# Performance work log

Measured on AMD Instinct MI355X. Metric: run time of the kernel, lower is better.

Reference implementation:

```python
import jax, jax.numpy as jnp
import numpy as np

# static config (mirrors init_kwargs)
F_T, S = 8, 24            # video_shape = (F_T, S, S)
K, DIL = 3, 1             # kernel_size, dilation (same for all 3 axes)
HEADS, DHEAD, DIM = 8, 64, 512
INNER = HEADS * DHEAD
PAD = DIL * (K - 1)       # causal: pad 2 at the FRONT of each spatial axis
KJ = K ** 3               # 27 neighbors per query
N_VID = F_T * S * S       # 4608 video tokens


def causal_pad(t):
    # t: [B, D, F, S, S] -> pad front of f/h/w axes (torch F.pad (PAD*?,0) causal layout)
    return jnp.pad(t, ((0, 0), (0, 0), (PAD, 0), (PAD, 0), (PAD, 0)))


def unfold3d(t):
    # torch unfoldNd equivalent. t: [B, D, F+PAD, S+PAD, S+PAD]
    # returns [B, N_VID, KJ, D]; kernel offsets ordered (kf, kh, kw) w fastest,
    # matching torch unfold's channel-major / kernel-minor layout after the
    # rearrange 'b (d j) i -> b i j d'.
    sl = []
    for i in range(K):
        for j in range(K):
            for kk in range(K):
                sl.append(t[:, :, i * DIL:i * DIL + F_T,
                                  j * DIL:j * DIL + S,
                                  kk * DIL:kk * DIL + S])
    u = jnp.stack(sl, axis=2)                      # [B, D, KJ, F, S, S]
    B, D = t.shape[0], t.shape[1]
    u = u.reshape(B, D, KJ, N_VID)
    return jnp.transpose(u, (0, 3, 2, 1))          # [B, N_VID, KJ, D]


def make_mask():
    # True where the neighbor falls into zero padding (out-of-range / future under causal pad)
    ones = jnp.ones((1, 1, F_T, S, S), jnp.float32)
    u = unfold3d(causal_pad(ones))[0, :, :, 0]     # [N_VID, KJ]
    m = u == 0.0
    return jnp.pad(m, ((0, 0), (1, 0)), constant_values=False)  # bos col never masked


def stable_softmax(t, alpha=32.0 ** 2):
    t = t / alpha
    t = t - jax.lax.stop_gradient(jnp.max(t, axis=-1, keepdims=True))
    return jax.nn.softmax(t * alpha, axis=-1)


def setup_inputs() -> dict:
    key = jax.random.key(0)
    ks = jax.random.split(key, 9)
    return {
        "x": jax.random.normal(ks[0], (1, N_VID + 1, DIM), jnp.float32),
        "Wq": jax.random.normal(ks[1], (DIM, INNER), jnp.float32) * 0.02,
        "Wkv": jax.random.normal(ks[2], (DIM, 2 * INNER), jnp.float32) * 0.02,
        "W_th": jax.random.normal(ks[3], (HEADS, HEADS), jnp.float32) * 0.2,
        "Wout": jax.random.normal(ks[4], (INNER, DIM), jnp.float32) * 0.02,
        "bout": jax.random.normal(ks[5], (DIM,), jnp.float32) * 0.02,
        "ax1": jax.random.normal(ks[6], (K, HEADS), jnp.float32),
        "ax2": jax.random.normal(ks[7], (K, HEADS), jnp.float32),
        "ax3": jax.random.normal(ks[8], (K, HEADS), jnp.float32),
    }


def reference(x, Wq, Wkv, W_th, Wout, bout, ax1, ax2, ax3):
    b, n, _ = x.shape                       # b=1, n = 1 + N_VID (no extra padding)
    h, d = HEADS, DHEAD
    scale = d ** -0.5

    q = x @ Wq
    k, v = jnp.split(x @ Wkv, 2, axis=-1)

    def to_heads(t):  # 'b n (h d) -> (b h) n d'
        return t.reshape(b, n, h, d).transpose(0, 2, 1, 3).reshape(b * h, n, d)

    q, k, v = map(to_heads, (q, k, v))
    q = q[:, 1:] * scale                    # drop bos query
    k_bos, v_bos = k[:, :1], v[:, :1]       # [bh, 1, d]
    k, v = k[:, 1:], v[:, 1:]

    def to_vid(t):  # 'b (f h w) d -> b d f h w'
        return t.reshape(b * h, F_T, S, S, d).transpose(0, 4, 1, 2, 3)

    ku = unfold3d(causal_pad(to_vid(k)))    # [bh, N, KJ, d]
    vu = unfold3d(causal_pad(to_vid(v)))
    N = ku.shape[1]

    kb = jnp.broadcast_to(k_bos[:, :, None, :], (b * h, N, 1, d))
    vb = jnp.broadcast_to(v_bos[:, :, None, :], (b * h, N, 1, d))
    ku = jnp.concatenate([kb, ku], axis=2)  # [bh, N, KJ+1, d]
    vu = jnp.concatenate([vb, vu], axis=2)

    sim = jnp.einsum('bid,bijd->bij', q, ku)                 # [bh, N, KJ+1]

    # axial relative position bias over the 3x3x3 kernel, pad 0 for bos column
    rel = (ax1[:, None, None, :] + ax2[None, :, None, :] + ax3[None, None, :, :])
    rel = rel.reshape(KJ, h)                                 # [27, h]
    bias = jnp.pad(rel.T[:, None, :], ((0, 0), (0, 0), (1, 0)))  # [h, 1, KJ+1]

    sim = sim.reshape(b, h, N, KJ + 1) + bias[None]
    mask = make_mask()                                       # [N, KJ+1]
    sim = jnp.where(mask[None, None], -jnp.finfo(sim.dtype).max, sim)

    attn = stable_softmax(sim)                               # [b, h, N, KJ+1]
    attn = jnp.einsum('hg,bgij->bhij', W_th, attn)           # talking heads 1x1 conv

    out = jnp.einsum('bhij,bhijd->bhid', attn, vu.reshape(b, h, N, KJ + 1, d))
    out = jnp.concatenate([v_bos.reshape(b, h, 1, d), out], axis=2)  # re-attach bos value
    out = out.transpose(0, 2, 1, 3).reshape(b, n, h * d)     # '(b h) n d -> b n (h d)'
    return out @ Wout + bout
```

## Files before the change

kernel.cpp:

```cpp
#include <hip/hip_runtime.h>
#include <hip/hip_bf16.h>


constexpr int TFR   = 8;
constexpr int SDIM  = 24;
constexpr int NVID  = TFR * SDIM * SDIM;
constexpr int NTOK  = NVID + 1;
constexpr int NH    = 8;
constexpr int DM    = 512;
constexpr int NJ    = 28;

typedef __attribute__((ext_vector_type(8))) short bf16x8;
typedef __attribute__((ext_vector_type(8))) unsigned short ushort8;
typedef __attribute__((ext_vector_type(4))) float f32x4;

typedef const __attribute__((address_space(1))) unsigned int* gas_ptr;
typedef __attribute__((address_space(3))) unsigned int* las_ptr;

__device__ __forceinline__ float bf2f(unsigned short u) {
    return __uint_as_float((unsigned)u << 16);
}
__device__ __forceinline__ unsigned short f2bf(float f) {
    __hip_bfloat16 h = __float2bfloat16(f);
    return reinterpret_cast<unsigned short&>(h);
}

__global__ __launch_bounds__(256)
void prep_w(const float* __restrict__ Wq, const float* __restrict__ Wkv,
            const float* __restrict__ Wout, const float* __restrict__ x,
            __hip_bfloat16* __restrict__ Wqkvt, __hip_bfloat16* __restrict__ Woutt,
            __hip_bfloat16* __restrict__ xb)
{
    const int tid = threadIdx.x;
    int tb = blockIdx.x;

    if (tb >= 1024) {
        const size_t base = (size_t)(tb - 1024) * 2048 + (size_t)tid * 8;
        if (base < (size_t)NTOK * DM) {
            const float4 f0 = *(const float4*)(x + base);
            const float4 f1 = *(const float4*)(x + base + 4);
            unsigned short v[8] = { f2bf(f0.x), f2bf(f0.y), f2bf(f0.z), f2bf(f0.w),
                                    f2bf(f1.x), f2bf(f1.y), f2bf(f1.z), f2bf(f1.w) };
            *(ushort8*)(xb + base) = *(const ushort8*)v;
        }
        return;
    }

    __shared__ float t[32][33];
    const float* W; __hip_bfloat16* Wt; int Nd, tX, rowOff;
    if (tb < 256)      { W = Wq;   Wt = Wqkvt; Nd = 512;  tX = 16; rowOff = 0;   }
    else if (tb < 768) { tb -= 256; W = Wkv;  Wt = Wqkvt; Nd = 1024; tX = 32; rowOff = 512; }
    else               { tb -= 768; W = Wout; Wt = Woutt; Nd = 512;  tX = 16; rowOff = 0;   }
    const int n0 = (tb % tX) * 32, k0 = (tb / tX) * 32;
    const int r  = tid >> 3;
    const int c4 = (tid & 7) * 4;
    const float4 v = *(const float4*)(W + (size_t)(k0 + r) * Nd + n0 + c4);
    t[r][c4 + 0] = v.x; t[r][c4 + 1] = v.y; t[r][c4 + 2] = v.z; t[r][c4 + 3] = v.w;
    __syncthreads();
    #pragma unroll
    for (int j = 0; j < 4; ++j)
        Wt[(size_t)(rowOff + n0 + r) * 512 + k0 + c4 + j] = __float2bfloat16(t[c4 + j][r]);
}

__global__ __launch_bounds__(256)
void gemm_qkv(const __hip_bfloat16* __restrict__ Ab, const __hip_bfloat16* __restrict__ Bt,
              float* __restrict__ Cq, __hip_bfloat16* __restrict__ Ckv, int M)
{
    constexpr int BM = 128, BN = 128, BK = 64, K = 512;
    __shared__ __align__(16) short As[2][BM * BK];
    __shared__ __align__(16) short Bs[2][BN * BK];

    const int tid  = threadIdx.x;
    const int bid  = blockIdx.x;
    const int xcd  = bid & 7, pos = bid >> 3;
    const int L    = (xcd < 4) ? xcd * 56 + pos : 224 + (xcd - 4) * 55 + pos;
    const int m0   = (L / 12) * BM;
    const int n0   = (L % 12) * BN;

    const int lane = tid & 63;
    const int wave = tid >> 6;
    const int wm   = (wave >> 1) * 64;
    const int wn   = (wave & 1) * 64;
    const int col  = lane & 15;
    const int quad = lane >> 4;

    f32x4 acc[4][4] = {};

    auto stage = [&](int buf, int k0) {
        #pragma unroll
        for (int it = 0; it < 4; ++it) {
            const int idx = it * 256 + tid;
            const int r   = idx >> 3;
            const int u   = (idx & 7) ^ (r & 7);
            const int gm  = (m0 + r < M) ? (m0 + r) : (M - 1);
            const __hip_bfloat16* gp = Ab + (size_t)gm * K + k0 + u * 8;
            __builtin_amdgcn_global_load_lds(
                (gas_ptr)gp, (las_ptr)&As[buf][(it * 256 + wave * 64) * 8], 16, 0, 0);
        }
        #pragma unroll
        for (int it = 0; it < 4; ++it) {
            const int idx = it * 256 + tid;
            const int r   = idx >> 3;
            const int u   = (idx & 7) ^ (r & 7);
            const __hip_bfloat16* gp = Bt + (size_t)(n0 + r) * K + k0 + u * 8;
            __builtin_amdgcn_global_load_lds(
                (gas_ptr)gp, (las_ptr)&Bs[buf][(it * 256 + wave * 64) * 8], 16, 0, 0);
        }
    };

    stage(0, 0);
    __syncthreads();

    #pragma unroll 2
    for (int t = 0; t < K / BK; ++t) {
        const int cur = t & 1;
        if (t + 1 < K / BK) stage(cur ^ 1, (t + 1) * BK);

        #pragma unroll
        for (int ks = 0; ks < 2; ++ks) {
            bf16x8 af[4], bfr[4];
            #pragma unroll
            for (int mt = 0; mt < 4; ++mt) {
                const int r = wm + mt * 16 + col;
                const int u = (ks * 4 + quad) ^ (r & 7);
                af[mt] = *(const bf16x8*)(&As[cur][r * BK + u * 8]);
            }
            #pragma unroll
            for (int nt = 0; nt < 4; ++nt) {
                const int r = wn + nt * 16 + col;
                const int u = (ks * 4 + quad) ^ (r & 7);
                bfr[nt] = *(const bf16x8*)(&Bs[cur][r * BK + u * 8]);
            }
            #pragma unroll
            for (int mt = 0; mt < 4; ++mt)
                #pragma unroll
                for (int nt = 0; nt < 4; ++nt)
                    acc[mt][nt] = __builtin_amdgcn_mfma_f32_16x16x32_bf16(
                        af[mt], bfr[nt], acc[mt][nt], 0, 0, 0);
        }
        __syncthreads();
    }

    const bool isQ = (n0 < 512);
    #pragma unroll
    for (int mt = 0; mt < 4; ++mt) {
        #pragma unroll
        for (int r = 0; r < 4; ++r) {
            const int row = m0 + wm + mt * 16 + quad * 4 + r;
            if (row >= M) continue;
            #pragma unroll
            for (int nt = 0; nt < 4; ++nt) {
                const int cg = n0 + wn + nt * 16 + col;
                const float v = acc[mt][nt][r];
                if (isQ) Cq[(size_t)row * 512 + cg] = v * 0.125f;
                else     Ckv[(size_t)row * 1024 + (cg - 512)] = __float2bfloat16(v);
            }
        }
    }
}

__global__ __launch_bounds__(256)
void gemm_out(const __hip_bfloat16* __restrict__ A, const __hip_bfloat16* __restrict__ Bt,
              float* __restrict__ C, int M, const float* __restrict__ bias)
{
    constexpr int BM = 64, BN = 64, BK = 64, K = 512;
    __shared__ __align__(16) short As[2][BM * BK];
    __shared__ __align__(16) short Bs[2][BN * BK];

    const int tid  = threadIdx.x;
    const int bid  = blockIdx.x;
    const int L    = (bid & 7) * 73 + (bid >> 3);
    const int m0   = (L >> 3) * BM;
    const int n0   = (L & 7) * BN;
    const int lane = tid & 63;
    const int wave = tid >> 6;
    const int wm   = (wave >> 1) * 32;
    const int wn   = (wave & 1) * 32;
    const int col  = lane & 15;
    const int quad = lane >> 4;

    f32x4 acc[2][2] = {};

    auto stage = [&](int buf, int k0) {
        #pragma unroll
        for (int it = 0; it < 2; ++it) {
            const int idx = it * 256 + tid;
            const int r   = idx >> 3;
            const int u   = (idx & 7) ^ (r & 7);
            const int gm  = (m0 + r < M) ? (m0 + r) : (M - 1);
            const __hip_bfloat16* gp = A + (size_t)gm * K + k0 + u * 8;
            __builtin_amdgcn_global_load_lds(
                (gas_ptr)gp, (las_ptr)&As[buf][(it * 256 + wave * 64) * 8], 16, 0, 0);
        }
        #pragma unroll
        for (int it = 0; it < 2; ++it) {
            const int idx = it * 256 + tid;
            const int r   = idx >> 3;
            const int u   = (idx & 7) ^ (r & 7);
            const __hip_bfloat16* gp = Bt + (size_t)(n0 + r) * K + k0 + u * 8;
            __builtin_amdgcn_global_load_lds(
                (gas_ptr)gp, (las_ptr)&Bs[buf][(it * 256 + wave * 64) * 8], 16, 0, 0);
        }
    };

    stage(0, 0);
    __syncthreads();

    #pragma unroll 2
    for (int t = 0; t < K / BK; ++t) {
        const int cur = t & 1;
        if (t + 1 < K / BK) stage(cur ^ 1, (t + 1) * BK);

        #pragma unroll
        for (int ks = 0; ks < 2; ++ks) {
            bf16x8 af[2], bfr[2];
            #pragma unroll
            for (int mt = 0; mt < 2; ++mt) {
                const int r = wm + mt * 16 + col;
                const int u = (ks * 4 + quad) ^ (r & 7);
                af[mt] = *(const bf16x8*)(&As[cur][r * BK + u * 8]);
            }
            #pragma unroll
            for (int nt = 0; nt < 2; ++nt) {
                const int r = wn + nt * 16 + col;
                const int u = (ks * 4 + quad) ^ (r & 7);
                bfr[nt] = *(const bf16x8*)(&Bs[cur][r * BK + u * 8]);
            }
            #pragma unroll
            for (int mt = 0; mt < 2; ++mt)
                #pragma unroll
                for (int nt = 0; nt < 2; ++nt)
                    acc[mt][nt] = __builtin_amdgcn_mfma_f32_16x16x32_bf16(
                        af[mt], bfr[nt], acc[mt][nt], 0, 0, 0);
        }
        __syncthreads();
    }

    #pragma unroll
    for (int mt = 0; mt < 2; ++mt) {
        #pragma unroll
        for (int r = 0; r < 4; ++r) {
            const int row = m0 + wm + mt * 16 + quad * 4 + r;
            if (row >= M) continue;
            #pragma unroll
            for (int nt = 0; nt < 2; ++nt) {
                const int cg = n0 + wn + nt * 16 + col;
                C[(size_t)row * 512 + cg] = acc[mt][nt][r] + bias[cg];
            }
        }
    }
}

__global__ __launch_bounds__(256)
void attn_v2(const float* __restrict__ Q, const __hip_bfloat16* __restrict__ KVb,
             __hip_bfloat16* __restrict__ O,
             const float* __restrict__ W_th,
             const float* __restrict__ ax1, const float* __restrict__ ax2,
             const float* __restrict__ ax3)
{
    __shared__ float attn_s[4][NH * NJ];
    __shared__ float mixed_s[4][NH * NJ];

    const int tid  = threadIdx.x;
    const int wave = tid >> 6;
    const int lane = tid & 63;
    const int g    = lane >> 3;
    const int s    = lane & 7;
    const int bsw  = (blockIdx.x & 7) * (NVID / 4 / 8) + (blockIdx.x >> 3);
    const int i    = __builtin_amdgcn_readfirstlane(bsw * 4 + (tid >> 6));
    const int qrow = i + 1;

    const int t  = i / (SDIM * SDIM);
    const int rm = i % (SDIM * SDIM);
    const int y  = rm / SDIM;
    const int x  = rm % SDIM;

    float qf[8];
    {
        const float4 q0 = *(const float4*)(Q + (size_t)qrow * DM + lane * 8);
        const float4 q1 = *(const float4*)(Q + (size_t)qrow * DM + lane * 8 + 4);
        qf[0] = q0.x; qf[1] = q0.y; qf[2] = q0.z; qf[3] = q0.w;
        qf[4] = q1.x; qf[5] = q1.y; qf[6] = q1.z; qf[7] = q1.w;
    }
    float a1[3], a2[3], a3[3];
    #pragma unroll
    for (int d = 0; d < 3; ++d) {
        a1[d] = ax1[d * NH + g];
        a2[d] = ax2[d * NH + g];
        a3[d] = ax3[d * NH + g];
    }

    float sim[NJ];
    #pragma unroll
    for (int j = 0; j < NJ; ++j) {
        int row; bool valid; float bias;
        if (j == 0) { row = 0; valid = true; bias = 0.f; }
        else {
            const int jp = j - 1;
            const int di = jp / 9, dj = (jp / 3) % 3, dk = jp % 3;
            const int tt = t + di - 2, yy = y + dj - 2, xx = x + dk - 2;
            valid = (tt >= 0) && (yy >= 0) && (xx >= 0);
            row = 1 + tt * SDIM * SDIM + yy * SDIM + xx;
            bias = a1[di] + a2[dj] + a3[dk];
        }
        if (valid) {
            const ushort8 kv = *(const ushort8*)(KVb + (size_t)row * 1024 + lane * 8);
            float p = 0.f;
            #pragma unroll
            for (int e = 0; e < 8; ++e) p += bf2f(kv[e]) * qf[e];
            p += __shfl_xor(p, 1);
            p += __shfl_xor(p, 2);
            p += __shfl_xor(p, 4);
            sim[j] = p + bias;
        } else {
            sim[j] = -1e30f;
        }
    }

    float m = -1e30f;
    #pragma unroll
    for (int j = 0; j < NJ; ++j) m = fmaxf(m, sim[j]);
    float ssum = 0.f;
    #pragma unroll
    for (int j = 0; j < NJ; ++j) { sim[j] = __expf(sim[j] - m); ssum += sim[j]; }
    const float inv = 1.f / ssum;
    #pragma unroll
    for (int j = 0; j < NJ; ++j) sim[j] *= inv;

    if (s == 0) {
        #pragma unroll
        for (int u = 0; u < 7; ++u) {
            f32x4 v4 = { sim[4*u], sim[4*u+1], sim[4*u+2], sim[4*u+3] };
            *(f32x4*)(&attn_s[wave][g * NJ + 4 * u]) = v4;
        }
    }
    __syncthreads();

    if (tid < NH * NJ) {
        const int h = tid / NJ, j = tid % NJ;
        #pragma unroll
        for (int q = 0; q < 4; ++q) {
            float acc = 0.f;
            #pragma unroll
            for (int gg = 0; gg < NH; ++gg)
                acc += W_th[h * NH + gg] * attn_s[q][gg * NJ + j];
            mixed_s[q][h * NJ + j] = acc;
        }
    }
    __syncthreads();

    float acc8[8] = {};
    #pragma unroll
    for (int j = 0; j < NJ; ++j) {
        int row; bool valid;
        if (j == 0) { row = 0; valid = true; }
        else {
            const int jp = j - 1;
            const int di = jp / 9, dj = (jp / 3) % 3, dk = jp % 3;
            const int tt = t + di - 2, yy = y + dj - 2, xx = x + dk - 2;
            valid = (tt >= 0) && (yy >= 0) && (xx >= 0);
            row = 1 + tt * SDIM * SDIM + yy * SDIM + xx;
        }
        if (valid) {
            const ushort8 vv = *(const ushort8*)(KVb + (size_t)row * 1024 + 512 + lane * 8);
            const float w = mixed_s[wave][g * NJ + j];
            #pragma unroll
            for (int e = 0; e < 8; ++e) acc8[e] += w * bf2f(vv[e]);
        }
    }

    unsigned short o[8];
    #pragma unroll
    for (int e = 0; e < 8; ++e) o[e] = f2bf(acc8[e]);
    *(ushort8*)(O + (size_t)qrow * DM + lane * 8) = *(const ushort8*)o;

    if (i == 0) {
        const ushort8 vb = *(const ushort8*)(KVb + 512 + lane * 8);
        *(ushort8*)(O + lane * 8) = vb;
    }
}

extern "C" void kernel_launch(void* const* d_in, const int* in_sizes, int n_in,
                              void* d_out, int out_size, void* d_ws, size_t ws_size,
                              hipStream_t stream)
{
    const float* x    = (const float*)d_in[0];
    const float* Wq   = (const float*)d_in[1];
    const float* Wkv  = (const float*)d_in[2];
    const float* W_th = (const float*)d_in[3];
    const float* Wout = (const float*)d_in[4];
    const float* bout = (const float*)d_in[5];
    const float* ax1  = (const float*)d_in[6];
    const float* ax2  = (const float*)d_in[7];
    const float* ax3  = (const float*)d_in[8];
    float* out = (float*)d_out;

    char* p = (char*)d_ws;
    float* Qf = (float*)p;                       p += (size_t)NTOK * DM * 4;
    __hip_bfloat16* KVb   = (__hip_bfloat16*)p;  p += (size_t)NTOK * 2 * DM * 2;
    __hip_bfloat16* Ob    = (__hip_bfloat16*)p;  p += (size_t)NTOK * DM * 2;
    __hip_bfloat16* Wqkvt = (__hip_bfloat16*)p;  p += (size_t)3 * DM * DM * 2;
    __hip_bfloat16* Woutt = (__hip_bfloat16*)p;  p += (size_t)DM * DM * 2;
    __hip_bfloat16* xb    = (__hip_bfloat16*)p;  p += (size_t)NTOK * DM * 2;

    const dim3 blk(256);

    prep_w<<<2177, blk, 0, stream>>>(Wq, Wkv, Wout, x, Wqkvt, Woutt, xb);

    gemm_qkv<<<444, blk, 0, stream>>>(xb, Wqkvt, Qf, KVb, NTOK);

    attn_v2<<<dim3(NVID / 4), blk, 0, stream>>>(Qf, KVb, Ob, W_th, ax1, ax2, ax3);

    gemm_out<<<584, blk, 0, stream>>>(Ob, Woutt, out, NTOK, bout);
}
```

Baseline: 132.2 us.

## Software-pipeline neighbor K/V loads in attention and relax GEMM barriers

The attention kernel now issues K (and later V) neighbor loads in batches of seven into double buffers, overlapping them with dot products and accumulation. The first V batch is prefetched before the softmax and talking-heads mixing. Invalid neighbors load row 0 unconditionally instead of branching. Both GEMMs replace __syncthreads with explicit vmcnt waits plus raw s_barrier, letting the next tile's async LDS loads stay in flight, and launch bounds request 3 blocks per SM. The risks are higher register pressure and correctness depending on hand-counted vmcnt values.

```diff
diff --git a/kernel.cpp b/kernel.cpp
--- a/kernel.cpp
+++ b/kernel.cpp
@@ -109,12 +109,17 @@
     };
 
     stage(0, 0);
-    __syncthreads();
-
-    #pragma unroll 2
+
+    #pragma unroll
     for (int t = 0; t < K / BK; ++t) {
         const int cur = t & 1;
-        if (t + 1 < K / BK) stage(cur ^ 1, (t + 1) * BK);
+        if (t + 1 < K / BK) {
+            stage(cur ^ 1, (t + 1) * BK);
+            asm volatile("s_waitcnt vmcnt(8)" ::: "memory");
+        } else {
+            asm volatile("s_waitcnt vmcnt(0)" ::: "memory");
+        }
+        __builtin_amdgcn_s_barrier();
 
         #pragma unroll
         for (int ks = 0; ks < 2; ++ks) {
@@ -138,7 +143,7 @@
                     acc[mt][nt] = __builtin_amdgcn_mfma_f32_16x16x32_bf16(
                         af[mt], bfr[nt], acc[mt][nt], 0, 0, 0);
         }
-        __syncthreads();
+        __builtin_amdgcn_s_barrier();
     }
 
     const bool isQ = (n0 < 512);
@@ -204,12 +209,17 @@
     };
 
     stage(0, 0);
-    __syncthreads();
-
-    #pragma unroll 2
+
+    #pragma unroll
     for (int t = 0; t < K / BK; ++t) {
         const int cur = t & 1;
-        if (t + 1 < K / BK) stage(cur ^ 1, (t + 1) * BK);
+        if (t + 1 < K / BK) {
+            stage(cur ^ 1, (t + 1) * BK);
+            asm volatile("s_waitcnt vmcnt(4)" ::: "memory");
+        } else {
+            asm volatile("s_waitcnt vmcnt(0)" ::: "memory");
+        }
+        __builtin_amdgcn_s_barrier();
 
         #pragma unroll
         for (int ks = 0; ks < 2; ++ks) {
@@ -233,7 +243,7 @@
                     acc[mt][nt] = __builtin_amdgcn_mfma_f32_16x16x32_bf16(
                         af[mt], bfr[nt], acc[mt][nt], 0, 0, 0);
         }
-        __syncthreads();
+        __builtin_amdgcn_s_barrier();
     }
 
     #pragma unroll
@@ -251,8 +261,61 @@
     }
 }
 
-__global__ __launch_bounds__(256)
-void attn_v2(const float* __restrict__ Q, const __hip_bfloat16* __restrict__ KVb,
+__device__ __forceinline__ void neigh(int j, int t, int y, int x,
+                                      int& row, bool& val,
+                                      int& di, int& dj, int& dk)
+{
+    if (j == 0) { row = 0; val = true; di = 0; dj = 0; dk = 0; return; }
+    const int jp = j - 1;
+    di = jp / 9; dj = (jp / 3) % 3; dk = jp % 3;
+    const int tt = t + di - 2, yy = y + dj - 2, xx = x + dk - 2;
+    val = (tt >= 0) && (yy >= 0) && (xx >= 0);
+    row = val ? 1 + tt * SDIM * SDIM + yy * SDIM + xx : 0;
+}
+
+#define ISSUE_K(B, DST)                                                     \
+    { _Pragma("unroll")                                                     \
+      for (int u = 0; u < 7; ++u) {                                         \
+        int row; bool val; int di, dj, dk;                                  \
+        neigh((B) * 7 + u, t, y, x, row, val, di, dj, dk);                  \
+        DST[u] = *(const ushort8*)(KVb + (size_t)row * 1024 + lane * 8);    \
+      } }
+
+#define DOTS_K(B, SRC)                                                      \
+    { _Pragma("unroll")                                                     \
+      for (int u = 0; u < 7; ++u) {                                         \
+        const int j = (B) * 7 + u;                                          \
+        int row; bool val; int di, dj, dk;                                  \
+        neigh(j, t, y, x, row, val, di, dj, dk);                            \
+        float p = 0.f;                                                      \
+        _Pragma("unroll")                                                   \
+        for (int e = 0; e < 8; ++e) p += bf2f(SRC[u][e]) * qf[e];           \
+        p += __shfl_xor(p, 1);                                              \
+        p += __shfl_xor(p, 2);                                              \
+        p += __shfl_xor(p, 4);                                              \
+        sim[j] = !val ? -1e30f                                              \
+               : (j == 0 ? p : p + a1[di] + a2[dj] + a3[dk]);               \
+      } }
+
+#define ISSUE_V(B, DST)                                                     \
+    { _Pragma("unroll")                                                     \
+      for (int u = 0; u < 7; ++u) {                                         \
+        int row; bool val; int di, dj, dk;                                  \
+        neigh((B) * 7 + u, t, y, x, row, val, di, dj, dk);                  \
+        DST[u] = *(const ushort8*)(KVb + (size_t)row * 1024 + 512 + lane * 8); \
+      } }
+
+#define ACC_V(B, SRC)                                                       \
+    { _Pragma("unroll")                                                     \
+      for (int u = 0; u < 7; ++u) {                                         \
+        const int j = (B) * 7 + u;                                          \
+        const float w = mixed_s[wave][g * NJ + j];                          \
+        _Pragma("unroll")                                                   \
+        for (int e = 0; e < 8; ++e) acc8[e] += w * bf2f(SRC[u][e]);         \
+      } }
+
+__global__ __launch_bounds__(256, 3)
+void attn_v5(const float* __restrict__ Q, const __hip_bfloat16* __restrict__ KVb,
              __hip_bfloat16* __restrict__ O,
              const float* __restrict__ W_th,
              const float* __restrict__ ax1, const float* __restrict__ ax2,
@@ -267,7 +330,7 @@
     const int g    = lane >> 3;
     const int s    = lane & 7;
     const int bsw  = (blockIdx.x & 7) * (NVID / 4 / 8) + (blockIdx.x >> 3);
-    const int i    = __builtin_amdgcn_readfirstlane(bsw * 4 + (tid >> 6));
+    const int i    = __builtin_amdgcn_readfirstlane(bsw * 4 + wave);
     const int qrow = i + 1;
 
     const int t  = i / (SDIM * SDIM);
@@ -291,31 +354,17 @@
     }
 
     float sim[NJ];
-    #pragma unroll
-    for (int j = 0; j < NJ; ++j) {
-        int row; bool valid; float bias;
-        if (j == 0) { row = 0; valid = true; bias = 0.f; }
-        else {
-            const int jp = j - 1;
-            const int di = jp / 9, dj = (jp / 3) % 3, dk = jp % 3;
-            const int tt = t + di - 2, yy = y + dj - 2, xx = x + dk - 2;
-            valid = (tt >= 0) && (yy >= 0) && (xx >= 0);
-            row = 1 + tt * SDIM * SDIM + yy * SDIM + xx;
-            bias = a1[di] + a2[dj] + a3[dk];
-        }
-        if (valid) {
-            const ushort8 kv = *(const ushort8*)(KVb + (size_t)row * 1024 + lane * 8);
-            float p = 0.f;
-            #pragma unroll
-            for (int e = 0; e < 8; ++e) p += bf2f(kv[e]) * qf[e];
-            p += __shfl_xor(p, 1);
-            p += __shfl_xor(p, 2);
-            p += __shfl_xor(p, 4);
-            sim[j] = p + bias;
-        } else {
-            sim[j] = -1e30f;
-        }
-    }
+    ushort8 bufA[7], bufB[7];
+    ISSUE_K(0, bufA);
+    ISSUE_K(1, bufB);
+    DOTS_K(0, bufA);
+    ISSUE_K(2, bufA);
+    DOTS_K(1, bufB);
+    ISSUE_K(3, bufB);
+    DOTS_K(2, bufA);
+    DOTS_K(3, bufB);
+
+    ISSUE_V(0, bufA);
 
     float m = -1e30f;
     #pragma unroll
@@ -334,7 +383,8 @@
             *(f32x4*)(&attn_s[wave][g * NJ + 4 * u]) = v4;
         }
     }
-    __syncthreads();
+    asm volatile("s_waitcnt lgkmcnt(0)" ::: "memory");
+    __builtin_amdgcn_s_barrier();
 
     if (tid < NH * NJ) {
         const int h = tid / NJ, j = tid % NJ;
@@ -347,27 +397,17 @@
             mixed_s[q][h * NJ + j] = acc;
         }
     }
-    __syncthreads();
+    asm volatile("s_waitcnt lgkmcnt(0)" ::: "memory");
+    __builtin_amdgcn_s_barrier();
 
     float acc8[8] = {};
-    #pragma unroll
-    for (int j = 0; j < NJ; ++j) {
-        int row; bool valid;
-        if (j == 0) { row = 0; valid = true; }
-        else {
-            const int jp = j - 1;
-            const int di = jp / 9, dj = (jp / 3) % 3, dk = jp % 3;
-            const int tt = t + di - 2, yy = y + dj - 2, xx = x + dk - 2;
-            valid = (tt >= 0) && (yy >= 0) && (xx >= 0);
-            row = 1 + tt * SDIM * SDIM + yy * SDIM + xx;
-        }
-        if (valid) {
-            const ushort8 vv = *(const ushort8*)(KVb + (size_t)row * 1024 + 512 + lane * 8);
-            const float w = mixed_s[wave][g * NJ + j];
-            #pragma unroll
-            for (int e = 0; e < 8; ++e) acc8[e] += w * bf2f(vv[e]);
-        }
-    }
+    ISSUE_V(1, bufB);
+    ACC_V(0, bufA);
+    ISSUE_V(2, bufA);
+    ACC_V(1, bufB);
+    ISSUE_V(3, bufB);
+    ACC_V(2, bufA);
+    ACC_V(3, bufB);
 
     unsigned short o[8];
     #pragma unroll
@@ -375,8 +415,8 @@
     *(ushort8*)(O + (size_t)qrow * DM + lane * 8) = *(const ushort8*)o;
 
     if (i == 0) {
-        const ushort8 vb = *(const ushort8*)(KVb + 512 + lane * 8);
-        *(ushort8*)(O + lane * 8) = vb;
+        const ushort8 vb0 = *(const ushort8*)(KVb + 512 + lane * 8);
+        *(ushort8*)(O + lane * 8) = vb0;
     }
 }
 
@@ -409,7 +449,7 @@
 
     gemm_qkv<<<444, blk, 0, stream>>>(xb, Wqkvt, Qf, KVb, NTOK);
 
-    attn_v2<<<dim3(NVID / 4), blk, 0, stream>>>(Qf, KVb, Ob, W_th, ax1, ax2, ax3);
+    attn_v5<<<dim3(NVID / 4), blk, 0, stream>>>(Qf, KVb, Ob, W_th, ax1, ax2, ax3);
 
     gemm_out<<<584, blk, 0, stream>>>(Ob, Woutt, out, NTOK, bout);
 }
```

New measurement: 121.9 us. 7.8% less time.
